# Performance work log

Measured on AMD Instinct MI355X. Metric: run time of the kernel, lower is better.

The kernel has to match this reference:

```python
import jax, jax.numpy as jnp
import numpy as np

N_LAYERS, D_MODEL, H, D_K, D_V, D_FF, VOCAB = 6, 512, 8, 64, 64, 2048, 32000
B, S = 4, 512
NEG_INF = -jnp.inf


def positional_encoding(seq_len, d_model):
    # Faithful to the (buggy-vs-paper) source: angle = pos / 10000**(2*i/d_model),
    # sin for even i, cos for odd i (i is the raw channel index).
    pos = jnp.arange(seq_len, dtype=jnp.float32)[:, None]
    i = jnp.arange(d_model, dtype=jnp.float32)[None, :]
    angle = pos / jnp.power(10000.0, 2.0 * i / d_model)
    return jnp.where((jnp.arange(d_model) % 2 == 0)[None, :], jnp.sin(angle), jnp.cos(angle))


def layer_norm(x, g, b, eps=1e-5):
    mu = jnp.mean(x, -1, keepdims=True)
    var = jnp.mean((x - mu) ** 2, -1, keepdims=True)
    return (x - mu) * jax.lax.rsqrt(var + eps) * g + b


def mha(q_in, k_in, v_in, wq, wk, wv, wo, q_mask, k_mask, causal):
    # wq/wk: (H, D, D_K), wv: (H, D, D_V), wo: (H*D_V, D)
    q = jnp.einsum('bsd,hdk->bhsk', q_in, wq)
    k = jnp.einsum('btd,hdk->bhtk', k_in, wk)
    v = jnp.einsum('btd,hdk->bhtk', v_in, wv)
    scores = jnp.einsum('bhsk,bhtk->bhst', q, k) / jnp.sqrt(jnp.float32(D_K))
    allowed = q_mask[:, None, :, None] & k_mask[:, None, None, :]  # (B,1,S,T)
    if causal:
        sl, tl = q_in.shape[1], k_in.shape[1]
        allowed = allowed & (jnp.arange(tl)[None, :] <= jnp.arange(sl)[:, None])[None, None]
    scores = jnp.where(allowed, scores, NEG_INF)
    attn = jax.nn.softmax(scores, axis=-1)
    out = jnp.einsum('bhst,bhtk->bshk', attn, v)  # (B,S,H,D_V)
    out = out.reshape(out.shape[0], out.shape[1], H * D_V)
    return out @ wo


def ffn(x, w1, b1, w2, b2):
    return jax.nn.relu(x @ w1 + b1) @ w2 + b2


def setup_inputs() -> dict:
    key = jax.random.key(0)
    ks = iter(jax.random.split(key, 40))
    f = lambda shape, scale: (jax.random.normal(next(ks), shape, dtype=jnp.float32) * scale)
    inp = {
        'src_tokens': jax.random.randint(next(ks), (B, S), 0, VOCAB),
        'tgt_tokens': jax.random.randint(next(ks), (B, S), 0, VOCAB),
        'src_mask': jnp.ones((B, S), dtype=bool),
        'tgt_mask': jnp.ones((B, S), dtype=bool),
        'embed': f((VOCAB, D_MODEL), 0.02),
        'enc_wqkv': f((N_LAYERS, 3, H, D_MODEL, D_K), 0.04),
        'enc_wo': f((N_LAYERS, H * D_V, D_MODEL), 0.04),
        'enc_ff_w1': f((N_LAYERS, D_MODEL, D_FF), 0.02),
        'enc_ff_b1': jnp.zeros((N_LAYERS, D_FF), jnp.float32),
        'enc_ff_w2': f((N_LAYERS, D_FF, D_MODEL), 0.02),
        'enc_ff_b2': jnp.zeros((N_LAYERS, D_MODEL), jnp.float32),
        'enc_ln_g': jnp.ones((N_LAYERS, 2, D_MODEL), jnp.float32),
        'enc_ln_b': jnp.zeros((N_LAYERS, 2, D_MODEL), jnp.float32),
        'dec_wqkv1': f((N_LAYERS, 3, H, D_MODEL, D_K), 0.04),
        'dec_wo1': f((N_LAYERS, H * D_V, D_MODEL), 0.04),
        'dec_wqkv2': f((N_LAYERS, 3, H, D_MODEL, D_K), 0.04),
        'dec_wo2': f((N_LAYERS, H * D_V, D_MODEL), 0.04),
        'dec_ff_w1': f((N_LAYERS, D_MODEL, D_FF), 0.02),
        'dec_ff_b1': jnp.zeros((N_LAYERS, D_FF), jnp.float32),
        'dec_ff_w2': f((N_LAYERS, D_FF, D_MODEL), 0.02),
        'dec_ff_b2': jnp.zeros((N_LAYERS, D_MODEL), jnp.float32),
        'dec_ln_g': jnp.ones((N_LAYERS, 3, D_MODEL), jnp.float32),
        'dec_ln_b': jnp.zeros((N_LAYERS, 3, D_MODEL), jnp.float32),
        'out_w': f((D_MODEL, VOCAB), 0.02),
        'out_b': jnp.zeros((VOCAB,), jnp.float32),
    }
    return inp


def reference(src_tokens, tgt_tokens, src_mask, tgt_mask, embed,
              enc_wqkv, enc_wo, enc_ff_w1, enc_ff_b1, enc_ff_w2, enc_ff_b2, enc_ln_g, enc_ln_b,
              dec_wqkv1, dec_wo1, dec_wqkv2, dec_wo2, dec_ff_w1, dec_ff_b1, dec_ff_w2, dec_ff_b2,
              dec_ln_g, dec_ln_b, out_w, out_b):
    pe = positional_encoding(src_tokens.shape[1], D_MODEL)
    x = embed[src_tokens] + pe[None]
    for i in range(N_LAYERS):
        a = mha(x, x, x, enc_wqkv[i, 0], enc_wqkv[i, 1], enc_wqkv[i, 2], enc_wo[i], src_mask, src_mask, False)
        x = layer_norm(x + a, enc_ln_g[i, 0], enc_ln_b[i, 0])
        x = layer_norm(x + ffn(x, enc_ff_w1[i], enc_ff_b1[i], enc_ff_w2[i], enc_ff_b2[i]), enc_ln_g[i, 1], enc_ln_b[i, 1])
    pe_t = positional_encoding(tgt_tokens.shape[1], D_MODEL)
    y = embed[tgt_tokens] + pe_t[None]
    for i in range(N_LAYERS):
        a = mha(y, y, y, dec_wqkv1[i, 0], dec_wqkv1[i, 1], dec_wqkv1[i, 2], dec_wo1[i], tgt_mask, tgt_mask, True)
        y = layer_norm(y + a, dec_ln_g[i, 0], dec_ln_b[i, 0])
        a = mha(y, x, x, dec_wqkv2[i, 0], dec_wqkv2[i, 1], dec_wqkv2[i, 2], dec_wo2[i], tgt_mask, src_mask, False)
        y = layer_norm(y + a, dec_ln_g[i, 1], dec_ln_b[i, 1])
        y = layer_norm(y + ffn(y, dec_ff_w1[i], dec_ff_b1[i], dec_ff_w2[i], dec_ff_b2[i]), dec_ln_g[i, 2], dec_ln_b[i, 2])
    return y @ out_w + out_b
```

## Files before the change

kernel.cpp:

```cpp
#include <hip/hip_runtime.h>
#include <math.h>


typedef unsigned short u16;
typedef __attribute__((ext_vector_type(8))) short short8;
typedef __attribute__((ext_vector_type(4))) float f32x4;

__device__ __forceinline__ u16 f2bf(float f){
  unsigned u = __float_as_uint(f);
  return (u16)((u + 0x7fffu + ((u >> 16) & 1u)) >> 16);
}

#define GLDS16(gp, lp) __builtin_amdgcn_global_load_lds( \
    (const __attribute__((address_space(1))) unsigned int*)(const void*)(gp), \
    (__attribute__((address_space(3))) unsigned int*)(void*)(lp), 16, 0, 0)

__global__ __launch_bounds__(256) void embed_pe_kernel(
    const int* __restrict__ tok, const float* __restrict__ emb,
    float* __restrict__ out, u16* __restrict__ outh)
{
  int row = blockIdx.x;
  int s = row & 511;
  int t = tok[row];
  #pragma unroll
  for (int j = 0; j < 2; j++){
    int d = threadIdx.x + 256*j;
    float ang = (float)s * powf(10000.0f, -2.0f*(float)d/512.0f);
    float pe = (d & 1) ? cosf(ang) : sinf(ang);
    float v = emb[(size_t)t*512 + d] + pe;
    out[(size_t)row*512 + d] = v;
    outh[(size_t)row*512 + d] = f2bf(v);
  }
}

struct WDesc { const float* W; unsigned long long gs, ds; u16* dst; int K; int nx; int end; };
struct WPack { WDesc d[6]; };

__global__ __launch_bounds__(256) void wcast_multi(WPack P, int nseg){
  int blk = blockIdx.x, s = 0;
  while (s < nseg-1 && blk >= P.d[s].end) s++;
  WDesc D = P.d[s];
  int base = s ? P.d[s-1].end : 0;
  int lb = blk - base;
  int g = lb % D.nx, kt = lb / D.nx;
  __shared__ u16 T[64][65];
  int tid = threadIdx.x;
  const float* Wb = D.W + (size_t)g*D.gs + (size_t)kt*64*D.ds;
  #pragma unroll
  for (int i = 0; i < 16; i++){
    int li = tid + 256*i;
    int kk = li >> 6, c = li & 63;
    T[kk][c] = f2bf(Wb[(size_t)kk*D.ds + c]);
  }
  __syncthreads();
  #pragma unroll
  for (int i = 0; i < 16; i++){
    int lo = tid + 256*i;
    int c = lo >> 6, kk = lo & 63;
    D.dst[(size_t)(g*64 + c)*D.K + kt*64 + kk] = T[kk][c];
  }
}

__global__ __launch_bounds__(256) void flash_attn_kernel(
    const u16* __restrict__ qkv, const u16* __restrict__ vT,
    u16* __restrict__ ctx, int causal)
{
  __shared__ __align__(16) u16 lQ[64*64];
  __shared__ __align__(16) u16 lK[2][64*64];
  __shared__ __align__(16) u16 lV[2][64*64];
  __shared__ __align__(16) u16 lP[4][16*64];
  int tid = threadIdx.x, lane = tid & 63, w = tid >> 6;
  int r16 = lane & 15, l4 = lane >> 4;
  int bh = blockIdx.x >> 3, qb = blockIdx.x & 7;
  int b = bh >> 3, h = bh & 7;
  const u16* qbase = qkv + (size_t)b*512*1536 + h*64;

  #pragma unroll
  for (int i = 0; i < 2; i++){
    int idx = i*256 + tid;
    int r = idx >> 3, c = idx & 7;
    GLDS16(qbase + (size_t)(qb*64 + r)*1536 + ((c ^ (r & 7))*8),
           lQ + (i*256 + w*64)*8);
  }
  auto stageKV = [&](int buf, int tt){
    #pragma unroll
    for (int i = 0; i < 2; i++){
      int idx = i*256 + tid;
      int r = idx >> 3, c = idx & 7;
      GLDS16(qbase + 512 + (size_t)(tt*64 + r)*1536 + ((c ^ (r & 7))*8),
             lK[buf] + (i*256 + w*64)*8);
      GLDS16(vT + ((size_t)bh*64 + r)*512 + tt*64 + ((c ^ (r & 7))*8),
             lV[buf] + (i*256 + w*64)*8);
    }
  };
  stageKV(0, 0);
  __syncthreads();
  short8 qa[2];
  #pragma unroll
  for (int kt = 0; kt < 2; kt++){
    int q = w*16 + r16;
    qa[kt] = *(const short8*)&lQ[q*64 + (((kt*4 + l4) ^ (q & 7))*8)];
  }

  f32x4 o[4];
  float mrow[4], lrow[4];
  #pragma unroll
  for (int j = 0; j < 4; j++){ o[j] = (f32x4){0.f,0.f,0.f,0.f}; mrow[j] = -3e38f; lrow[j] = 0.f; }

  int ntl = causal ? (qb + 1) : 8;
  int buf = 0;
  for (int tt = 0; tt < ntl; tt++){
    if (tt + 1 < ntl) stageKV(buf ^ 1, tt + 1);
    f32x4 s[4];
    #pragma unroll
    for (int ct = 0; ct < 4; ct++) s[ct] = (f32x4){0.f,0.f,0.f,0.f};
    __builtin_amdgcn_s_setprio(1);
    #pragma unroll
    for (int kt = 0; kt < 2; kt++){
      #pragma unroll
      for (int ct = 0; ct < 4; ct++){
        int trow = ct*16 + r16;
        short8 kb = *(const short8*)&lK[buf][trow*64 + (((kt*4 + l4) ^ (trow & 7))*8)];
        s[ct] = __builtin_amdgcn_mfma_f32_16x16x32_bf16(qa[kt], kb, s[ct], 0, 0, 0);
      }
    }
    __builtin_amdgcn_s_setprio(0);
    float p[4][4];
    #pragma unroll
    for (int ct = 0; ct < 4; ct++)
      #pragma unroll
      for (int r = 0; r < 4; r++){
        float v = s[ct][r] * 0.125f;
        if (causal && tt == qb && (ct*16 + r16) > (w*16 + l4*4 + r)) v = -1e30f;
        p[ct][r] = v;
      }
    #pragma unroll
    for (int r = 0; r < 4; r++){
      float pm = fmaxf(fmaxf(p[0][r], p[1][r]), fmaxf(p[2][r], p[3][r]));
      #pragma unroll
      for (int off = 1; off < 16; off <<= 1) pm = fmaxf(pm, __shfl_xor(pm, off));
      float mn = fmaxf(mrow[r], pm);
      float scl = __expf(mrow[r] - mn);
      mrow[r] = mn;
      float rs = 0.f;
      #pragma unroll
      for (int ct = 0; ct < 4; ct++){ p[ct][r] = __expf(p[ct][r] - mn); rs += p[ct][r]; }
      #pragma unroll
      for (int off = 1; off < 16; off <<= 1) rs += __shfl_xor(rs, off);
      lrow[r] = lrow[r]*scl + rs;
      #pragma unroll
      for (int jf = 0; jf < 4; jf++) o[jf][r] *= scl;
    }
    u16* myP = &lP[w][0];
    #pragma unroll
    for (int ct = 0; ct < 4; ct++)
      #pragma unroll
      for (int r = 0; r < 4; r++){
        int q = l4*4 + r, t = ct*16 + r16;
        myP[q*64 + (((t >> 3) ^ (q & 7))*8) + (t & 7)] = f2bf(p[ct][r]);
      }
    __builtin_amdgcn_s_setprio(1);
    #pragma unroll
    for (int kt = 0; kt < 2; kt++){
      short8 pa = *(const short8*)&myP[r16*64 + (((kt*4 + l4) ^ (r16 & 7))*8)];
      #pragma unroll
      for (int jf = 0; jf < 4; jf++){
        int dr = jf*16 + r16;
        short8 vv = *(const short8*)&lV[buf][dr*64 + (((kt*4 + l4) ^ (dr & 7))*8)];
        o[jf] = __builtin_amdgcn_mfma_f32_16x16x32_bf16(pa, vv, o[jf], 0, 0, 0);
      }
    }
    __builtin_amdgcn_s_setprio(0);
    __syncthreads();
    buf ^= 1;
  }
  #pragma unroll
  for (int r = 0; r < 4; r++){
    float inv = 1.0f / lrow[r];
    int q = qb*64 + w*16 + l4*4 + r;
    u16* dst = ctx + (size_t)(b*512 + q)*512 + h*64;
    #pragma unroll
    for (int jf = 0; jf < 4; jf++)
      dst[jf*16 + r16] = f2bf(o[jf][r] * inv);
  }
}

__global__ __launch_bounds__(256) void ln_kernel(
    float* __restrict__ x, const float* __restrict__ res,
    const float* __restrict__ g, const float* __restrict__ bt,
    u16* __restrict__ xh)
{
  int tid = threadIdx.x, lane = tid & 63, wv = tid >> 6;
  int row = blockIdx.x*4 + wv;
  size_t base = (size_t)row*512;
  float v[8]; float sum = 0.f;
  #pragma unroll
  for (int j = 0; j < 8; j++){
    int d = lane + 64*j;
    v[j] = x[base + d] + res[base + d];
    sum += v[j];
  }
  #pragma unroll
  for (int o = 32; o; o >>= 1) sum += __shfl_xor(sum, o);
  float mu = sum * (1.0f/512.0f);
  float vs = 0.f;
  #pragma unroll
  for (int j = 0; j < 8; j++){ float dd = v[j] - mu; vs += dd*dd; }
  #pragma unroll
  for (int o = 32; o; o >>= 1) vs += __shfl_xor(vs, o);
  float rstd = rsqrtf(vs*(1.0f/512.0f) + 1e-5f);
  #pragma unroll
  for (int j = 0; j < 8; j++){
    int d = lane + 64*j;
    float ov = (v[j] - mu)*rstd*g[d] + bt[d];
    x[base + d] = ov;
    xh[base + d] = f2bf(ov);
  }
}

template<int BM, int BN, int WM, int WN, int VOUT>
__global__ __launch_bounds__(WM*WN*64) void mfma_gemm(
    const u16* __restrict__ A, int lda,
    const u16* __restrict__ B, int ldb,
    void* __restrict__ C, int ldc, int cbf,
    const float* __restrict__ bias, int relu, int K, u16* __restrict__ vt)
{
  constexpr int NT  = WM*WN*64;
  constexpr int SM  = BM/WM, SN = BN/WN;
  constexpr int FM  = SM/16, FN = SN/16;
  constexpr int RPS = NT/8;
  constexpr int AG  = BM/RPS, BG = BN/RPS;
  __shared__ __align__(16) u16 lds[2][(BM+BN)*64];
  int tid = threadIdx.x, lane = tid & 63, w = tid >> 6;
  int wm = w / WN, wn = w % WN;
  int r16 = lane & 15, l4 = lane >> 4;
  int sr = (w << 3) + (lane >> 3);
  int sc = lane & 7;
  int scs = sc ^ (sr & 7);
  const u16* Ab = A + (size_t)blockIdx.y*BM*lda + (size_t)sr*lda + scs*8;
  const u16* Bb = B + (size_t)blockIdx.x*BN*ldb + (size_t)sr*ldb + scs*8;
  f32x4 acc[FM][FN];
  #pragma unroll
  for (int i = 0; i < FM; i++)
    #pragma unroll
    for (int j = 0; j < FN; j++)
      acc[i][j] = (f32x4){0.f, 0.f, 0.f, 0.f};

  auto stage = [&](int buf, int kt){
    #pragma unroll
    for (int s = 0; s < AG; s++)
      GLDS16(Ab + (size_t)(s*RPS)*lda + kt, &lds[buf][(s*RPS + (w << 3))*64]);
    #pragma unroll
    for (int s = 0; s < BG; s++)
      GLDS16(Bb + (size_t)(s*RPS)*ldb + kt, &lds[buf][(BM + s*RPS + (w << 3))*64]);
  };
  stage(0, 0);
  int nk = K >> 6, cur = 0;
  for (int kt = 0; kt < nk; kt++){
    __syncthreads();
    if (kt + 1 < nk) stage(cur ^ 1, (kt + 1) << 6);
    #pragma unroll
    for (int ks = 0; ks < 2; ks++){
      short8 av[FM], bv[FN];
      #pragma unroll
      for (int i = 0; i < FM; i++){
        int row = wm*SM + i*16 + r16;
        av[i] = *(const short8*)&lds[cur][row*64 + (((ks*4 + l4) ^ (row & 7))*8)];
      }
      #pragma unroll
      for (int j = 0; j < FN; j++){
        int row = wn*SN + j*16 + r16;
        bv[j] = *(const short8*)&lds[cur][(BM + row)*64 + (((ks*4 + l4) ^ (row & 7))*8)];
      }
      #pragma unroll
      for (int i = 0; i < FM; i++)
        #pragma unroll
        for (int j = 0; j < FN; j++)
          acc[i][j] = __builtin_amdgcn_mfma_f32_16x16x32_bf16(av[i], bv[j], acc[i][j], 0, 0, 0);
    }
    cur ^= 1;
  }

  if constexpr (VOUT){
    int nblk = blockIdx.x * BN;
    if (nblk >= 1024){
      constexpr int TP = BM + 4;
      u16* T = &lds[0][0];
      __syncthreads();
      #pragma unroll
      for (int i = 0; i < FM; i++){
        int t0 = wm*SM + i*16 + l4*4;
        #pragma unroll
        for (int j = 0; j < FN; j++){
          int d = wn*SN + j*16 + r16;
          unsigned q01 = (unsigned)f2bf(acc[i][j][0]) | ((unsigned)f2bf(acc[i][j][1]) << 16);
          unsigned q23 = (unsigned)f2bf(acc[i][j][2]) | ((unsigned)f2bf(acc[i][j][3]) << 16);
          uint2 pk; pk.x = q01; pk.y = q23;
          *(uint2*)&T[d*TP + t0] = pk;
        }
      }
      __syncthreads();
      int h0 = (nblk - 1024) >> 6;
      int b = (blockIdx.y * BM) >> 9;
      int t0g = (blockIdx.y * BM) & 511;
      constexpr int U2PR = BM/4;
      constexpr int NIT = (BN*BM)/(NT*4);
      #pragma unroll
      for (int it = 0; it < NIT; it++){
        int idx = it*NT + tid;
        int d = idx / U2PR, tq = (idx % U2PR)*4;
        int hh = d >> 6, dd = d & 63;
        *(uint2*)&vt[((size_t)((b*8 + h0 + hh)*64 + dd))*512 + t0g + tq] =
            *(const uint2*)&T[d*TP + tq];
      }
      return;
    }
  }

  int m0 = blockIdx.y*BM + wm*SM, n0 = blockIdx.x*BN + wn*SN;
  int r4 = l4*4;
  #pragma unroll
  for (int i = 0; i < FM; i++){
    #pragma unroll
    for (int j = 0; j < FN; j++){
      int col = n0 + j*16 + r16;
      float bi = bias ? bias[col] : 0.f;
      #pragma unroll
      for (int r = 0; r < 4; r++){
        int rowg = m0 + i*16 + r4 + r;
        float o = acc[i][j][r] + bi;
        if (relu) o = fmaxf(o, 0.f);
        if (cbf) ((u16*)C)[(size_t)rowg*ldc + col] = f2bf(o);
        else     ((float*)C)[(size_t)rowg*ldc + col] = o;
      }
    }
  }
}

__global__ __launch_bounds__(256) void xattn_qkv_gemm(
    const u16* __restrict__ Ay, const u16* __restrict__ Ax,
    const u16* __restrict__ Bt, u16* __restrict__ C, u16* __restrict__ vt)
{
  constexpr int BM=64, BN=64, WM=2, WN=2, NT=256;
  constexpr int SM=BM/WM, SN=BN/WN, FM=SM/16, FN=SN/16, RPS=NT/8;
  constexpr int AG=BM/RPS, BG=BN/RPS;
  __shared__ __align__(16) u16 lA[2][BM*64];
  __shared__ __align__(16) u16 lB[2][BN*64];
  int tid = threadIdx.x, lane = tid & 63, w = tid >> 6;
  int wm = w / WN, wn = w % WN;
  int r16 = lane & 15, l4 = lane >> 4;
  int sr = (w << 3) + (lane >> 3);
  int sc = lane & 7;
  int scs = sc ^ (sr & 7);
  int z = blockIdx.z;
  const u16* A = (z == 0) ? Ay : Ax;
  const u16* Ab = A + (size_t)blockIdx.y*BM*512 + (size_t)sr*512 + scs*8;
  const u16* Bb = Bt + (size_t)(z*512 + blockIdx.x*BN)*512 + (size_t)sr*512 + scs*8;
  f32x4 acc[FM][FN];
  #pragma unroll
  for (int i = 0; i < FM; i++)
    #pragma unroll
    for (int j = 0; j < FN; j++)
      acc[i][j] = (f32x4){0.f, 0.f, 0.f, 0.f};
  auto stage = [&](int buf, int kt){
    #pragma unroll
    for (int s = 0; s < AG; s++)
      GLDS16(Ab + (size_t)(s*RPS)*512 + kt, &lA[buf][(s*RPS + (w << 3))*64]);
    #pragma unroll
    for (int s = 0; s < BG; s++)
      GLDS16(Bb + (size_t)(s*RPS)*512 + kt, &lB[buf][(s*RPS + (w << 3))*64]);
  };
  stage(0, 0);
  int cur = 0;
  for (int kt = 0; kt < 8; kt++){
    __syncthreads();
    if (kt + 1 < 8) stage(cur ^ 1, (kt + 1) << 6);
    #pragma unroll
    for (int ks = 0; ks < 2; ks++){
      short8 av[FM], bv[FN];
      #pragma unroll
      for (int i = 0; i < FM; i++){
        int row = wm*SM + i*16 + r16;
        av[i] = *(const short8*)&lA[cur][row*64 + (((ks*4 + l4) ^ (row & 7))*8)];
      }
      #pragma unroll
      for (int j = 0; j < FN; j++){
        int row = wn*SN + j*16 + r16;
        bv[j] = *(const short8*)&lB[cur][row*64 + (((ks*4 + l4) ^ (row & 7))*8)];
      }
      #pragma unroll
      for (int i = 0; i < FM; i++)
        #pragma unroll
        for (int j = 0; j < FN; j++)
          acc[i][j] = __builtin_amdgcn_mfma_f32_16x16x32_bf16(av[i], bv[j], acc[i][j], 0, 0, 0);
    }
    cur ^= 1;
  }
  if (z == 2){
    constexpr int TP = BM + 4;
    u16* T = (u16*)&lA[0][0];
    __syncthreads();
    #pragma unroll
    for (int i = 0; i < FM; i++){
      int t0 = wm*SM + i*16 + l4*4;
      #pragma unroll
      for (int j = 0; j < FN; j++){
        int d = wn*SN + j*16 + r16;
        unsigned q01 = (unsigned)f2bf(acc[i][j][0]) | ((unsigned)f2bf(acc[i][j][1]) << 16);
        unsigned q23 = (unsigned)f2bf(acc[i][j][2]) | ((unsigned)f2bf(acc[i][j][3]) << 16);
        uint2 pk; pk.x = q01; pk.y = q23;
        *(uint2*)&T[d*TP + t0] = pk;
      }
    }
    __syncthreads();
    int h = blockIdx.x;
    int b = (blockIdx.y * BM) >> 9;
    int t0g = (blockIdx.y * BM) & 511;
    u16* dst = vt + (size_t)(b*8 + h)*64*512;
    #pragma unroll
    for (int it = 0; it < (BM*64)/(NT*4); it++){
      int idx = it*NT + tid;
      int d = idx >> 4, tq = (idx & 15)*4;
      *(uint2*)&dst[(size_t)d*512 + t0g + tq] = *(const uint2*)&T[d*TP + tq];
    }
    return;
  }
  int m0 = blockIdx.y*BM + wm*SM, n0 = z*512 + blockIdx.x*BN + wn*SN;
  int r4 = l4*4;
  #pragma unroll
  for (int i = 0; i < FM; i++)
    #pragma unroll
    for (int j = 0; j < FN; j++)
      #pragma unroll
      for (int r = 0; r < 4; r++){
        int rowg = m0 + i*16 + r4 + r;
        C[(size_t)rowg*1536 + n0 + j*16 + r16] = f2bf(acc[i][j][r]);
      }
}

extern "C" void kernel_launch(void* const* d_in, const int* in_sizes, int n_in,
                              void* d_out, int out_size, void* d_ws, size_t ws_size,
                              hipStream_t stream)
{
  (void)in_sizes; (void)n_in; (void)out_size; (void)ws_size;
  const int*   src_tok   = (const int*)  d_in[0];
  const int*   tgt_tok   = (const int*)  d_in[1];
  const float* emb       = (const float*)d_in[4];
  const float* enc_wqkv  = (const float*)d_in[5];
  const float* enc_wo    = (const float*)d_in[6];
  const float* enc_ff_w1 = (const float*)d_in[7];
  const float* enc_ff_b1 = (const float*)d_in[8];
  const float* enc_ff_w2 = (const float*)d_in[9];
  const float* enc_ff_b2 = (const float*)d_in[10];
  const float* enc_ln_g  = (const float*)d_in[11];
  const float* enc_ln_b  = (const float*)d_in[12];
  const float* dec_wqkv1 = (const float*)d_in[13];
  const float* dec_wo1   = (const float*)d_in[14];
  const float* dec_wqkv2 = (const float*)d_in[15];
  const float* dec_wo2   = (const float*)d_in[16];
  const float* dec_ff_w1 = (const float*)d_in[17];
  const float* dec_ff_b1 = (const float*)d_in[18];
  const float* dec_ff_w2 = (const float*)d_in[19];
  const float* dec_ff_b2 = (const float*)d_in[20];
  const float* dec_ln_g  = (const float*)d_in[21];
  const float* dec_ln_b  = (const float*)d_in[22];
  const float* out_w     = (const float*)d_in[23];
  const float* out_b     = (const float*)d_in[24];
  float* outp = (float*)d_out;

  const size_t MB = 1024*1024;
  char* wsb = (char*)d_ws;
  float* xb     = (float*)(wsb + 0*MB);
  u16*   sQKV2  = (u16*)  (wsb + 0*MB);
  u16*   sWO2   = (u16*)  (wsb + 1*MB + 512*1024);
  float* yb     = (float*)(wsb + 4*MB);
  u16*   xh     = (u16*)  (wsb + 8*MB);
  u16*   ctxb   = (u16*)  (wsb + 10*MB);
  u16*   yh     = (u16*)  (wsb + 12*MB);
  u16*   qkvb   = (u16*)  (wsb + 14*MB);
  u16*   vT     = (u16*)  (wsb + 20*MB);
  u16*   hid    = (u16*)  (wsb + 14*MB);
  u16*   sQKV   = (u16*)  (wsb + 22*MB);
  u16*   sWO    = (u16*)  (wsb + 23*MB + 512*1024);
  u16*   sFF1   = (u16*)  (wsb + 24*MB);
  u16*   sFF2   = (u16*)  (wsb + 26*MB);
  float* proj   = (float*)(wsb + 28*MB);
  u16*   wvbuf  = (u16*)  (wsb + 0*MB);

  auto g64 = [&](const u16* A,int lda,const u16* B,int ldb,void* C,int ldc,
                 int cbf,const float* bias,int relu,int M,int N,int K){
    mfma_gemm<64,64,2,2,0><<<dim3(N/64, M/64), 256, 0, stream>>>(
        A,lda,B,ldb,C,ldc,cbf,bias,relu,K,nullptr);
  };
  auto g128 = [&](const u16* A,int lda,const u16* B,int ldb,void* C,int ldc,
                  int cbf,const float* bias,int relu,int M,int N,int K){
    mfma_gemm<128,128,2,2,0><<<dim3(N/128, M/128), 256, 0, stream>>>(
        A,lda,B,ldb,C,ldc,cbf,bias,relu,K,nullptr);
  };
  auto gqkv = [&](const u16* A,const u16* B,u16* C,u16* vt){
    mfma_gemm<128,128,2,2,1><<<dim3(12, 16), 256, 0, stream>>>(
        A,512,B,512,C,1536,1,nullptr,0,512,vt);
  };
  auto ln = [&](float* x, const float* g, const float* b, u16* oh){
    ln_kernel<<<512, 256, 0, stream>>>(x, proj, g, b, oh);
  };
  auto cast = [&](WDesc* segs, int n){
    WPack P; int tot = 0;
    for (int s = 0; s < n; s++){
      tot += segs[s].nx * (segs[s].K/64);
      segs[s].end = tot;
      P.d[s] = segs[s];
    }
    for (int s = n; s < 6; s++) P.d[s] = P.d[0];
    wcast_multi<<<tot, 256, 0, stream>>>(P, n);
  };

  const size_t WQKV_L = (size_t)3*8*512*64;

  embed_pe_kernel<<<2048, 256, 0, stream>>>(src_tok, emb, xb, xh);
  for (int i = 0; i < 6; i++){
    WDesc segs[4] = {
      {enc_wqkv + i*WQKV_L,            32768, 64,   sQKV, 512,  24, 0},
      {enc_wo   + (size_t)i*262144,    64,    512,  sWO,  512,  8,  0},
      {enc_ff_w1+ (size_t)i*512*2048,  64,    2048, sFF1, 512,  32, 0},
      {enc_ff_w2+ (size_t)i*2048*512,  64,    512,  sFF2, 2048, 8,  0}};
    cast(segs, 4);
    gqkv(xh, sQKV, qkvb, vT);
    flash_attn_kernel<<<256, 256, 0, stream>>>(qkvb, vT, ctxb, 0);
    g64(ctxb, 512, sWO, 512, proj, 512, 0, nullptr, 0, 2048, 512, 512);
    ln(xb, enc_ln_g + i*1024,       enc_ln_b + i*1024,       xh);
    g128(xh, 512, sFF1, 512, hid, 2048, 1, enc_ff_b1 + i*2048, 1, 2048, 2048, 512);
    g64(hid, 2048, sFF2, 2048, proj, 512, 0, enc_ff_b2 + i*512, 0, 2048, 512, 2048);
    ln(xb, enc_ln_g + i*1024 + 512, enc_ln_b + i*1024 + 512, xh);
  }

  embed_pe_kernel<<<2048, 256, 0, stream>>>(tgt_tok, emb, yb, yh);
  for (int i = 0; i < 6; i++){
    WDesc segs[6] = {
      {dec_wqkv1 + i*WQKV_L,           32768, 64,   sQKV,  512,  24, 0},
      {dec_wo1   + (size_t)i*262144,   64,    512,  sWO,   512,  8,  0},
      {dec_ff_w1 + (size_t)i*512*2048, 64,    2048, sFF1,  512,  32, 0},
      {dec_ff_w2 + (size_t)i*2048*512, 64,    512,  sFF2,  2048, 8,  0},
      {dec_wqkv2 + i*WQKV_L,           32768, 64,   sQKV2, 512,  24, 0},
      {dec_wo2   + (size_t)i*262144,   64,    512,  sWO2,  512,  8,  0}};
    cast(segs, 6);
    gqkv(yh, sQKV, qkvb, vT);
    flash_attn_kernel<<<256, 256, 0, stream>>>(qkvb, vT, ctxb, 1);
    g64(ctxb, 512, sWO, 512, proj, 512, 0, nullptr, 0, 2048, 512, 512);
    ln(yb, dec_ln_g + i*1536,        dec_ln_b + i*1536,        yh);
    xattn_qkv_gemm<<<dim3(8, 32, 3), 256, 0, stream>>>(yh, xh, sQKV2, qkvb, vT);
    flash_attn_kernel<<<256, 256, 0, stream>>>(qkvb, vT, ctxb, 0);
    g64(ctxb, 512, sWO2, 512, proj, 512, 0, nullptr, 0, 2048, 512, 512);
    ln(yb, dec_ln_g + i*1536 + 512,  dec_ln_b + i*1536 + 512,  yh);
    g128(yh, 512, sFF1, 512, hid, 2048, 1, dec_ff_b1 + i*2048, 1, 2048, 2048, 512);
    g64(hid, 2048, sFF2, 2048, proj, 512, 0, dec_ff_b2 + i*512, 0, 2048, 512, 2048);
    ln(yb, dec_ln_g + i*1536 + 1024, dec_ln_b + i*1536 + 1024, yh);
  }

  const int c0s[4] = {0, 11776, 23552, 32000};
  for (int c = 0; c < 3; c++){
    int c0 = c0s[c], NC = c0s[c+1] - c0;
    WDesc seg[1] = {{out_w + c0, 64, 32000, wvbuf, 512, NC/64, 0}};
    cast(seg, 1);
    g128(yh, 512, wvbuf, 512, outp + c0, 32000, 0, out_b + c0, 0, 2048, NC, 512);
  }
}
```

Baseline: 1.459 ms.

## Fuse next-layer weight casts into LayerNorm launches and merge embedding kernels

```diff
diff --git a/kernel.cpp b/kernel.cpp
--- a/kernel.cpp
+++ b/kernel.cpp
@@ -15,13 +15,18 @@
     (const __attribute__((address_space(1))) unsigned int*)(const void*)(gp), \
     (__attribute__((address_space(3))) unsigned int*)(void*)(lp), 16, 0, 0)
 
-__global__ __launch_bounds__(256) void embed_pe_kernel(
-    const int* __restrict__ tok, const float* __restrict__ emb,
-    float* __restrict__ out, u16* __restrict__ outh)
-{
-  int row = blockIdx.x;
+__global__ __launch_bounds__(256) void embed_dual_kernel(
+    const int* __restrict__ src, const int* __restrict__ tgt,
+    const float* __restrict__ emb,
+    float* __restrict__ xb, u16* __restrict__ xh,
+    float* __restrict__ yb, u16* __restrict__ yh)
+{
+  int which = blockIdx.x >> 11;
+  int row = blockIdx.x & 2047;
   int s = row & 511;
-  int t = tok[row];
+  int t = which ? tgt[row] : src[row];
+  float* out = which ? yb : xb;
+  u16*  outh = which ? yh : xh;
   #pragma unroll
   for (int j = 0; j < 2; j++){
     int d = threadIdx.x + 256*j;
@@ -36,14 +41,14 @@
 struct WDesc { const float* W; unsigned long long gs, ds; u16* dst; int K; int nx; int end; };
 struct WPack { WDesc d[6]; };
 
-__global__ __launch_bounds__(256) void wcast_multi(WPack P, int nseg){
-  int blk = blockIdx.x, s = 0;
+__device__ __forceinline__ void cast_body(const WPack& P, int nseg, int blk){
+  __shared__ u16 T[64][65];
+  int s = 0;
   while (s < nseg-1 && blk >= P.d[s].end) s++;
   WDesc D = P.d[s];
   int base = s ? P.d[s-1].end : 0;
   int lb = blk - base;
   int g = lb % D.nx, kt = lb / D.nx;
-  __shared__ u16 T[64][65];
   int tid = threadIdx.x;
   const float* Wb = D.W + (size_t)g*D.gs + (size_t)kt*64*D.ds;
   #pragma unroll
@@ -59,6 +64,61 @@
     int c = lo >> 6, kk = lo & 63;
     D.dst[(size_t)(g*64 + c)*D.K + kt*64 + kk] = T[kk][c];
   }
+}
+
+__global__ __launch_bounds__(256) void wcast_multi(WPack P, int nseg){
+  cast_body(P, nseg, blockIdx.x);
+}
+
+__device__ __forceinline__ void ln_body(
+    float* __restrict__ x, const float* __restrict__ res,
+    const float* __restrict__ g, const float* __restrict__ bt,
+    u16* __restrict__ xh, int blk)
+{
+  int tid = threadIdx.x, lane = tid & 63, wv = tid >> 6;
+  int row = blk*4 + wv;
+  size_t base = (size_t)row*512;
+  float v[8]; float sum = 0.f;
+  #pragma unroll
+  for (int j = 0; j < 8; j++){
+    int d = lane + 64*j;
+    v[j] = x[base + d] + res[base + d];
+    sum += v[j];
+  }
+  #pragma unroll
+  for (int o = 32; o; o >>= 1) sum += __shfl_xor(sum, o);
+  float mu = sum * (1.0f/512.0f);
+  float vs = 0.f;
+  #pragma unroll
+  for (int j = 0; j < 8; j++){ float dd = v[j] - mu; vs += dd*dd; }
+  #pragma unroll
+  for (int o = 32; o; o >>= 1) vs += __shfl_xor(vs, o);
+  float rstd = rsqrtf(vs*(1.0f/512.0f) + 1e-5f);
+  #pragma unroll
+  for (int j = 0; j < 8; j++){
+    int d = lane + 64*j;
+    float ov = (v[j] - mu)*rstd*g[d] + bt[d];
+    x[base + d] = ov;
+    xh[base + d] = f2bf(ov);
+  }
+}
+
+__global__ __launch_bounds__(256) void ln_cast_kernel(
+    float* __restrict__ x, const float* __restrict__ res,
+    const float* __restrict__ g, const float* __restrict__ bt,
+    u16* __restrict__ xh, WPack P, int nseg)
+{
+  int bid = blockIdx.x;
+  if (bid < 512){ ln_body(x, res, g, bt, xh, bid); return; }
+  cast_body(P, nseg, bid - 512);
+}
+
+__global__ __launch_bounds__(256) void ln_kernel(
+    float* __restrict__ x, const float* __restrict__ res,
+    const float* __restrict__ g, const float* __restrict__ bt,
+    u16* __restrict__ xh)
+{
+  ln_body(x, res, g, bt, xh, blockIdx.x);
 }
 
 __global__ __launch_bounds__(256) void flash_attn_kernel(
@@ -182,39 +242,6 @@
     #pragma unroll
     for (int jf = 0; jf < 4; jf++)
       dst[jf*16 + r16] = f2bf(o[jf][r] * inv);
-  }
-}
-
-__global__ __launch_bounds__(256) void ln_kernel(
-    float* __restrict__ x, const float* __restrict__ res,
-    const float* __restrict__ g, const float* __restrict__ bt,
-    u16* __restrict__ xh)
-{
-  int tid = threadIdx.x, lane = tid & 63, wv = tid >> 6;
-  int row = blockIdx.x*4 + wv;
-  size_t base = (size_t)row*512;
-  float v[8]; float sum = 0.f;
-  #pragma unroll
-  for (int j = 0; j < 8; j++){
-    int d = lane + 64*j;
-    v[j] = x[base + d] + res[base + d];
-    sum += v[j];
-  }
-  #pragma unroll
-  for (int o = 32; o; o >>= 1) sum += __shfl_xor(sum, o);
-  float mu = sum * (1.0f/512.0f);
-  float vs = 0.f;
-  #pragma unroll
-  for (int j = 0; j < 8; j++){ float dd = v[j] - mu; vs += dd*dd; }
-  #pragma unroll
-  for (int o = 32; o; o >>= 1) vs += __shfl_xor(vs, o);
-  float rstd = rsqrtf(vs*(1.0f/512.0f) + 1e-5f);
-  #pragma unroll
-  for (int j = 0; j < 8; j++){
-    int d = lane + 64*j;
-    float ov = (v[j] - mu)*rstd*g[d] + bt[d];
-    x[base + d] = ov;
-    xh[base + d] = f2bf(ov);
   }
 }
 
@@ -485,7 +512,7 @@
   u16*   sFF1   = (u16*)  (wsb + 24*MB);
   u16*   sFF2   = (u16*)  (wsb + 26*MB);
   float* proj   = (float*)(wsb + 28*MB);
-  u16*   wvbuf  = (u16*)  (wsb + 0*MB);
+  u16*   wvbuf  = (u16*)  (wsb + 14*MB);
 
   auto g64 = [&](const u16* A,int lda,const u16* B,int ldb,void* C,int ldc,
                  int cbf,const float* bias,int relu,int M,int N,int K){
@@ -504,46 +531,62 @@
   auto ln = [&](float* x, const float* g, const float* b, u16* oh){
     ln_kernel<<<512, 256, 0, stream>>>(x, proj, g, b, oh);
   };
-  auto cast = [&](WDesc* segs, int n){
-    WPack P; int tot = 0;
+  auto packof = [&](WDesc* segs, int n, int& tot){
+    WPack P; tot = 0;
     for (int s = 0; s < n; s++){
       tot += segs[s].nx * (segs[s].K/64);
       segs[s].end = tot;
       P.d[s] = segs[s];
     }
     for (int s = n; s < 6; s++) P.d[s] = P.d[0];
+    return P;
+  };
+  auto cast = [&](WDesc* segs, int n){
+    int tot; WPack P = packof(segs, n, tot);
     wcast_multi<<<tot, 256, 0, stream>>>(P, n);
   };
+  auto ln_cast = [&](float* x, const float* g, const float* b, u16* oh,
+                     WDesc* segs, int n){
+    int tot; WPack P = packof(segs, n, tot);
+    ln_cast_kernel<<<512 + tot, 256, 0, stream>>>(x, proj, g, b, oh, P, n);
+  };
 
   const size_t WQKV_L = (size_t)3*8*512*64;
-
-  embed_pe_kernel<<<2048, 256, 0, stream>>>(src_tok, emb, xb, xh);
+  auto enc_segs = [&](int i, WDesc* s){
+    s[0] = {enc_wqkv + i*WQKV_L,            32768, 64,   sQKV, 512,  24, 0};
+    s[1] = {enc_wo   + (size_t)i*262144,    64,    512,  sWO,  512,  8,  0};
+    s[2] = {enc_ff_w1+ (size_t)i*512*2048,  64,    2048, sFF1, 512,  32, 0};
+    s[3] = {enc_ff_w2+ (size_t)i*2048*512,  64,    512,  sFF2, 2048, 8,  0};
+  };
+  auto dec_segs = [&](int i, WDesc* s){
+    s[0] = {dec_wqkv1 + i*WQKV_L,           32768, 64,   sQKV,  512,  24, 0};
+    s[1] = {dec_wo1   + (size_t)i*262144,   64,    512,  sWO,   512,  8,  0};
+    s[2] = {dec_ff_w1 + (size_t)i*512*2048, 64,    2048, sFF1,  512,  32, 0};
+    s[3] = {dec_ff_w2 + (size_t)i*2048*512, 64,    512,  sFF2,  2048, 8,  0};
+    s[4] = {dec_wqkv2 + i*WQKV_L,           32768, 64,   sQKV2, 512,  24, 0};
+    s[5] = {dec_wo2   + (size_t)i*262144,   64,    512,  sWO2,  512,  8,  0};
+  };
+
+  embed_dual_kernel<<<4096, 256, 0, stream>>>(src_tok, tgt_tok, emb, xb, xh, yb, yh);
+
+  { WDesc s[4]; enc_segs(0, s); cast(s, 4); }
   for (int i = 0; i < 6; i++){
-    WDesc segs[4] = {
-      {enc_wqkv + i*WQKV_L,            32768, 64,   sQKV, 512,  24, 0},
-      {enc_wo   + (size_t)i*262144,    64,    512,  sWO,  512,  8,  0},
-      {enc_ff_w1+ (size_t)i*512*2048,  64,    2048, sFF1, 512,  32, 0},
-      {enc_ff_w2+ (size_t)i*2048*512,  64,    512,  sFF2, 2048, 8,  0}};
-    cast(segs, 4);
     gqkv(xh, sQKV, qkvb, vT);
     flash_attn_kernel<<<256, 256, 0, stream>>>(qkvb, vT, ctxb, 0);
     g64(ctxb, 512, sWO, 512, proj, 512, 0, nullptr, 0, 2048, 512, 512);
-    ln(xb, enc_ln_g + i*1024,       enc_ln_b + i*1024,       xh);
+    ln(xb, enc_ln_g + i*1024, enc_ln_b + i*1024, xh);
     g128(xh, 512, sFF1, 512, hid, 2048, 1, enc_ff_b1 + i*2048, 1, 2048, 2048, 512);
     g64(hid, 2048, sFF2, 2048, proj, 512, 0, enc_ff_b2 + i*512, 0, 2048, 512, 2048);
-    ln(xb, enc_ln_g + i*1024 + 512, enc_ln_b + i*1024 + 512, xh);
-  }
-
-  embed_pe_kernel<<<2048, 256, 0, stream>>>(tgt_tok, emb, yb, yh);
+    if (i < 5){
+      WDesc s[4]; enc_segs(i+1, s);
+      ln_cast(xb, enc_ln_g + i*1024 + 512, enc_ln_b + i*1024 + 512, xh, s, 4);
+    } else {
+      ln(xb, enc_ln_g + i*1024 + 512, enc_ln_b + i*1024 + 512, xh);
+    }
+  }
+
+  { WDesc s[6]; dec_segs(0, s); cast(s, 6); }
   for (int i = 0; i < 6; i++){
-    WDesc segs[6] = {
-      {dec_wqkv1 + i*WQKV_L,           32768, 64,   sQKV,  512,  24, 0},
-      {dec_wo1   + (size_t)i*262144,   64,    512,  sWO,   512,  8,  0},
-      {dec_ff_w1 + (size_t)i*512*2048, 64,    2048, sFF1,  512,  32, 0},
-      {dec_ff_w2 + (size_t)i*2048*512, 64,    512,  sFF2,  2048, 8,  0},
-      {dec_wqkv2 + i*WQKV_L,           32768, 64,   sQKV2, 512,  24, 0},
-      {dec_wo2   + (size_t)i*262144,   64,    512,  sWO2,  512,  8,  0}};
-    cast(segs, 6);
     gqkv(yh, sQKV, qkvb, vT);
     flash_attn_kernel<<<256, 256, 0, stream>>>(qkvb, vT, ctxb, 1);
     g64(ctxb, 512, sWO, 512, proj, 512, 0, nullptr, 0, 2048, 512, 512);
@@ -554,14 +597,18 @@
     ln(yb, dec_ln_g + i*1536 + 512,  dec_ln_b + i*1536 + 512,  yh);
     g128(yh, 512, sFF1, 512, hid, 2048, 1, dec_ff_b1 + i*2048, 1, 2048, 2048, 512);
     g64(hid, 2048, sFF2, 2048, proj, 512, 0, dec_ff_b2 + i*512, 0, 2048, 512, 2048);
-    ln(yb, dec_ln_g + i*1536 + 1024, dec_ln_b + i*1536 + 1024, yh);
-  }
-
-  const int c0s[4] = {0, 11776, 23552, 32000};
-  for (int c = 0; c < 3; c++){
-    int c0 = c0s[c], NC = c0s[c+1] - c0;
-    WDesc seg[1] = {{out_w + c0, 64, 32000, wvbuf, 512, NC/64, 0}};
+    if (i < 5){
+      WDesc s[6]; dec_segs(i+1, s);
+      ln_cast(yb, dec_ln_g + i*1536 + 1024, dec_ln_b + i*1536 + 1024, yh, s, 6);
+    } else {
+      ln(yb, dec_ln_g + i*1536 + 1024, dec_ln_b + i*1536 + 1024, yh);
+    }
+  }
+
+  for (int c = 0; c < 2; c++){
+    int c0 = c*16000;
+    WDesc seg[1] = {{out_w + c0, 64, 32000, wvbuf, 512, 250, 0}};
     cast(seg, 1);
-    g128(yh, 512, wvbuf, 512, outp + c0, 32000, 0, out_b + c0, 0, 2048, NC, 512);
-  }
-}
+    g128(yh, 512, wvbuf, 512, outp + c0, 32000, 0, out_b + c0, 0, 2048, 16000, 512);
+  }
+}
```

Result: no change. 1.440 ms (-1.3%).
